# Kernel tuning notes

Measured on AMD Instinct MI355X. Metric: run time of the kernel, lower is better.

The kernel has to match this reference:

```python
import jax, jax.numpy as jnp
import numpy as np

N, IN_DIM, L, K, D = 131072, 128, 16, 8, 50
ENC_H, DEC_H, HEAD_H, DF = 64, 16, 64, 1.0


def setup_inputs() -> dict:
    key = jax.random.key(0)
    ks = jax.random.split(key, 20)
    s = lambda k, shape, fan: jax.random.normal(k, shape, jnp.float32) * (1.0 / np.sqrt(fan))
    return {
        "x": jax.random.normal(ks[0], (N, IN_DIM), jnp.float32),
        # encoder: in -> 64 -> 64 -> L
        "We1": s(ks[1], (IN_DIM, ENC_H), IN_DIM), "be1": jnp.zeros((ENC_H,), jnp.float32),
        "We2": s(ks[2], (ENC_H, ENC_H), ENC_H),   "be2": jnp.zeros((ENC_H,), jnp.float32),
        "We3": s(ks[3], (ENC_H, L), ENC_H),       "be3": jnp.zeros((L,), jnp.float32),
        # decoder: L -> 16 -> in
        "Wd1": s(ks[4], (L, DEC_H), L),           "bd1": jnp.zeros((DEC_H,), jnp.float32),
        "Wd2": s(ks[5], (DEC_H, IN_DIM), DEC_H),  "bd2": jnp.zeros((IN_DIM,), jnp.float32),
        # K per-cluster survival heads: (L+in) -> 64 -> num_durations
        "Wh1": s(ks[6], (K, L + IN_DIM, HEAD_H), L + IN_DIM), "bh1": jnp.zeros((K, HEAD_H), jnp.float32),
        "Wh2": s(ks[7], (K, HEAD_H, D), HEAD_H),              "bh2": jnp.zeros((K, D), jnp.float32),
        # cluster centers buffer
        "centers": jax.random.normal(ks[8], (K, L), jnp.float32) * 0.05,
    }


def _student_t_sim(z, centers, df):
    # z: [N, L], centers: [K, L] -> q: [N, K]
    dist2 = jnp.sum((z[:, None, :] - centers[None, :, :]) ** 2, axis=-1)
    logits = -0.5 * (df + 1.0) * jnp.log1p(dist2 / df)
    return jax.nn.softmax(logits, axis=1)


def reference(x, We1, be1, We2, be2, We3, be3, Wd1, bd1, Wd2, bd2,
              Wh1, bh1, Wh2, bh2, centers):
    relu = jax.nn.relu
    # encoder (eval mode: dropout off, non-variational)
    e = relu(x @ We1 + be1)
    e = relu(e @ We2 + be2)
    z = e @ We3 + be3                      # [N, L]
    q = _student_t_sim(z, centers, DF)     # [N, K]
    h = jnp.concatenate([z, x], axis=1)    # [N, L+in]
    # cluster-argmax routing to per-cluster heads: compute all K, select winner
    cluster_idx = jnp.argmax(q, axis=1)    # [N]
    h1 = relu(jnp.einsum("nf,kfh->nkh", h, Wh1) + bh1[None])   # [N, K, H]
    lg = jnp.einsum("nkh,khd->nkd", h1, Wh2) + bh2[None]       # [N, K, D]
    surv_logits = jnp.take_along_axis(lg, cluster_idx[:, None, None], axis=1)[:, 0]  # [N, D]
    # decoder + reconstruction loss per sample
    d = relu(z @ Wd1 + bd1)
    x_hat = d @ Wd2 + bd2                  # [N, in]
    rec_ps = jnp.mean((x_hat - x) ** 2, axis=1)
    kld = jnp.zeros((x.shape[0],), x.dtype)
    return z, q, surv_logits, x_hat, rec_ps, kld
```

## Files before the change

### kernel.cpp

```cpp
#include <hip/hip_runtime.h>

#define NS 131072
#define KC 8
typedef unsigned long long u64;

#define LD4(P) (*reinterpret_cast<const float4*>(&sm[(P)]))
#define ST4(P) (*reinterpret_cast<float4*>(&sm[(P)]))
#define GL4(P) (*reinterpret_cast<const float4*>(&(P)))

#define FMA4(ACCR, AV, B) do { \
  ACCR[0]=fmaf((AV),(B).x,ACCR[0]); ACCR[1]=fmaf((AV),(B).y,ACCR[1]); \
  ACCR[2]=fmaf((AV),(B).z,ACCR[2]); ACCR[3]=fmaf((AV),(B).w,ACCR[3]); } while(0)

#define K4(ACC, ABASE, ASTR, AK, BBASE, BSTR, JOFF, BK) do { \
  const float4 b0=LD4((BBASE)+((BK)*4+0)*(BSTR)+(JOFF)); \
  const float4 b1=LD4((BBASE)+((BK)*4+1)*(BSTR)+(JOFF)); \
  const float4 b2=LD4((BBASE)+((BK)*4+2)*(BSTR)+(JOFF)); \
  const float4 b3=LD4((BBASE)+((BK)*4+3)*(BSTR)+(JOFF)); \
  _Pragma("unroll") \
  for (int m_ = 0; m_ < 8; ++m_) { \
    const float4 av = LD4((ABASE)+(st+16*m_)*(ASTR)+(AK)*4); \
    FMA4(ACC[m_], av.x, b0); FMA4(ACC[m_], av.y, b1); \
    FMA4(ACC[m_], av.z, b2); FMA4(ACC[m_], av.w, b3); } \
} while(0)

#define INIT84(ACC, BPTR, OFF) do { \
  const float4 u_ = *reinterpret_cast<const float4*>(&(BPTR)[(OFF)]); \
  _Pragma("unroll") for (int m_=0;m_<8;++m_){ \
    ACC[m_][0]=u_.x; ACC[m_][1]=u_.y; ACC[m_][2]=u_.z; ACC[m_][3]=u_.w; } } while(0)

#define RELU84(ACC) do { _Pragma("unroll") for (int m_=0;m_<8;++m_) \
  { _Pragma("unroll") for (int j_=0;j_<4;++j_) ACC[m_][j_]=fmaxf(ACC[m_][j_],0.f); } } while(0)

#define WRITE_E(ACC) do { _Pragma("unroll") for (int m_=0;m_<8;++m_){ \
  ST4(AR + (st+16*m_)*68 + job) = \
    make_float4(ACC[m_][0],ACC[m_][1],ACC[m_][2],ACC[m_][3]); } } while(0)

#define STAGE_X() do { \
  ST4(AR + xr0*20 + xcc)     = rx0; \
  ST4(AR + xr0*20 + xcc + 4) = rx1; } while(0)

#define AR   0
#define WD1i 2560
#define WB   8704
#define SMW  9792

__global__ __launch_bounds__(256, 2) void k_enc(
    const float* __restrict__ x,
    const float* __restrict__ We1, const float* __restrict__ be1,
    const float* __restrict__ We2, const float* __restrict__ be2,
    const float* __restrict__ We3, const float* __restrict__ be3,
    const float* __restrict__ Wd1, const float* __restrict__ bd1,
    const float* __restrict__ Wd2, const float* __restrict__ bd2,
    const float* __restrict__ centers,
    float* __restrict__ out_z, float* __restrict__ out_q,
    float* __restrict__ xhat, float* __restrict__ rec, float* __restrict__ kld,
    int* __restrict__ cidx, int* __restrict__ counts)
{
    __shared__ float sm[SMW];
    const int t  = threadIdx.x;
    const int ot = t & 15, st = t >> 4;
    const int job = ot * 4;
    const int s0 = blockIdx.x * 128;
    const int xr0 = t >> 1, xcc = (t & 1) * 8;
    const int wr  = t >> 4, wc  = (t & 15) * 4;

    {
        float acc1[8][4];
        INIT84(acc1, be1, job);
        float4 rx0 = GL4(x[(size_t)(s0+xr0)*128 + xcc]);
        float4 rx1 = GL4(x[(size_t)(s0+xr0)*128 + xcc + 4]);
        float4 rw  = GL4(We1[(size_t)wr*64 + wc]);
        #pragma unroll 1
        for (int c = 0; c < 8; ++c) {
            __syncthreads();
            STAGE_X();
            ST4(WB + wr*68 + wc) = rw;
            __syncthreads();
            if (c < 7) {
                rx0 = GL4(x[(size_t)(s0+xr0)*128 + (c+1)*16 + xcc]);
                rx1 = GL4(x[(size_t)(s0+xr0)*128 + (c+1)*16 + xcc + 4]);
                rw  = GL4(We1[(size_t)((c+1)*16 + wr)*64 + wc]);
            }
            #pragma unroll
            for (int kc = 0; kc < 4; ++kc) K4(acc1, AR, 20, kc, WB, 68, job, kc);
        }
        __syncthreads();
        RELU84(acc1);
        WRITE_E(acc1);
    }

    {
        float acc2[8][4];
        INIT84(acc2, be2, job);
        float4 rw = GL4(We2[(size_t)wr*64 + wc]);
        #pragma unroll 1
        for (int c = 0; c < 4; ++c) {
            __syncthreads();
            ST4(WB + wr*68 + wc) = rw;
            __syncthreads();
            if (c < 3) rw = GL4(We2[(size_t)((c+1)*16 + wr)*64 + wc]);
            #pragma unroll
            for (int kc = 0; kc < 4; ++kc) K4(acc2, AR, 68, c*4 + kc, WB, 68, job, kc);
        }
        __syncthreads();
        RELU84(acc2);
        WRITE_E(acc2);
    }
    {   const int row = t >> 2, c4 = (t & 3) * 4;
        ST4(WB + row*16 + c4) = GL4(We3[(size_t)row*16 + c4]); }
    __syncthreads();

    float zac[8];
    {   const float b3v = be3[ot];
        #pragma unroll
        for (int m = 0; m < 8; ++m) zac[m] = b3v; }
    #pragma unroll 2
    for (int kc = 0; kc < 16; ++kc) {
        const float w0 = sm[WB + (kc*4+0)*16 + ot];
        const float w1 = sm[WB + (kc*4+1)*16 + ot];
        const float w2 = sm[WB + (kc*4+2)*16 + ot];
        const float w3 = sm[WB + (kc*4+3)*16 + ot];
        #pragma unroll
        for (int m = 0; m < 8; ++m) {
            const float4 av = LD4(AR + (st + 16*m)*68 + kc*4);
            float s = zac[m];
            s = fmaf(av.x, w0, s); s = fmaf(av.y, w1, s);
            s = fmaf(av.z, w2, s); s = fmaf(av.w, w3, s);
            zac[m] = s;
        }
    }
    #pragma unroll
    for (int m = 0; m < 8; ++m)
        out_z[(size_t)(s0 + st + 16*m)*16 + ot] = zac[m];
    __syncthreads();
    #pragma unroll
    for (int m = 0; m < 8; ++m) sm[AR + (st + 16*m)*20 + ot] = zac[m];
    ST4(WB + wr*68 + wc) = GL4(Wd2[(size_t)wr*128 + wc]);
    if (t < 64) ST4(WD1i + (t >> 2)*16 + (t & 3)*4) =
        GL4(Wd1[(t >> 2)*16 + (t & 3)*4]);
    __syncthreads();

    if (t < 128) {
        const float4 z0 = LD4(AR + t*20 + 0), z1 = LD4(AR + t*20 + 4);
        const float4 z2 = LD4(AR + t*20 + 8), z3 = LD4(AR + t*20 + 12);
        const float zz[16] = {z0.x,z0.y,z0.z,z0.w, z1.x,z1.y,z1.z,z1.w,
                              z2.x,z2.y,z2.z,z2.w, z3.x,z3.y,z3.z,z3.w};
        float d2[KC];
        #pragma unroll
        for (int k = 0; k < KC; ++k) {
            float acc = 0.f;
            #pragma unroll
            for (int l = 0; l < 16; ++l) {
                const float dl = zz[l] - centers[k*16 + l];
                acc = fmaf(dl, dl, acc);
            }
            d2[k] = acc;
        }
        float lgt[KC], ex[KC];
        float mm = -1e30f;
        #pragma unroll
        for (int k = 0; k < KC; ++k) { lgt[k] = -log1pf(d2[k]); mm = fmaxf(mm, lgt[k]); }
        float ssum = 0.f;
        #pragma unroll
        for (int k = 0; k < KC; ++k) { ex[k] = expf(lgt[k] - mm); ssum += ex[k]; }
        const float inv = 1.f / ssum;
        float4* oq = reinterpret_cast<float4*>(&out_q[(size_t)(s0 + t)*8]);
        oq[0] = make_float4(ex[0]*inv, ex[1]*inv, ex[2]*inv, ex[3]*inv);
        oq[1] = make_float4(ex[4]*inv, ex[5]*inv, ex[6]*inv, ex[7]*inv);
        int ci = 0; float best = d2[0];
        #pragma unroll
        for (int k = 1; k < KC; ++k) if (d2[k] < best) { best = d2[k]; ci = k; }
        cidx[s0 + t] = ci;
        #pragma unroll
        for (int k = 0; k < KC; ++k) {
            const u64 mk = __ballot(ci == k);
            if ((t & 63) == 0 && mk) atomicAdd(&counts[k], (int)__popcll(mk));
        }
        kld[s0 + t] = 0.f;
    }

    {
        float w[16];
        #pragma unroll
        for (int k = 0; k < 16; ++k) w[k] = sm[WD1i + k*16 + ot];
        const float bb = bd1[ot];
        float dac[8];
        #pragma unroll
        for (int m = 0; m < 8; ++m) {
            const int r = st + 16*m;
            float s = bb;
            #pragma unroll
            for (int kc = 0; kc < 4; ++kc) {
                const float4 av = LD4(AR + r*20 + kc*4);
                s = fmaf(av.x, w[kc*4+0], s); s = fmaf(av.y, w[kc*4+1], s);
                s = fmaf(av.z, w[kc*4+2], s); s = fmaf(av.w, w[kc*4+3], s);
            }
            dac[m] = fmaxf(s, 0.f);
        }
        __syncthreads();
        #pragma unroll
        for (int m = 0; m < 8; ++m) sm[AR + (st + 16*m)*20 + ot] = dac[m];
    }
    __syncthreads();

    float rp[8] = {0.f,0.f,0.f,0.f,0.f,0.f,0.f,0.f};
    float4 rw2 = GL4(Wd2[(size_t)wr*128 + 64 + wc]);
    {
        float accx[8][4];
        INIT84(accx, bd2, job);
        #pragma unroll
        for (int kc = 0; kc < 4; ++kc) K4(accx, AR, 20, kc, WB, 68, job, kc);
        #pragma unroll
        for (int m = 0; m < 8; ++m) {
            const int r = st + 16*m;
            const float4 xa = GL4(x[(size_t)(s0+r)*128 + job]);
            float df;
            df=accx[m][0]-xa.x; rp[m]=fmaf(df,df,rp[m]);
            df=accx[m][1]-xa.y; rp[m]=fmaf(df,df,rp[m]);
            df=accx[m][2]-xa.z; rp[m]=fmaf(df,df,rp[m]);
            df=accx[m][3]-xa.w; rp[m]=fmaf(df,df,rp[m]);
            *reinterpret_cast<float4*>(&xhat[(size_t)(s0+r)*128 + job]) =
                make_float4(accx[m][0],accx[m][1],accx[m][2],accx[m][3]);
        }
    }
    __syncthreads();
    ST4(WB + wr*68 + wc) = rw2;
    __syncthreads();
    {
        float accx[8][4];
        INIT84(accx, bd2, 64 + job);
        #pragma unroll
        for (int kc = 0; kc < 4; ++kc) K4(accx, AR, 20, kc, WB, 68, job, kc);
        #pragma unroll
        for (int m = 0; m < 8; ++m) {
            const int r = st + 16*m;
            const float4 xa = GL4(x[(size_t)(s0+r)*128 + 64 + job]);
            float df;
            df=accx[m][0]-xa.x; rp[m]=fmaf(df,df,rp[m]);
            df=accx[m][1]-xa.y; rp[m]=fmaf(df,df,rp[m]);
            df=accx[m][2]-xa.z; rp[m]=fmaf(df,df,rp[m]);
            df=accx[m][3]-xa.w; rp[m]=fmaf(df,df,rp[m]);
            *reinterpret_cast<float4*>(&xhat[(size_t)(s0+r)*128 + 64 + job]) =
                make_float4(accx[m][0],accx[m][1],accx[m][2],accx[m][3]);
        }
    }
    #pragma unroll
    for (int m = 0; m < 8; ++m) {
        float v = rp[m];
        v += __shfl_xor(v, 1); v += __shfl_xor(v, 2);
        v += __shfl_xor(v, 4); v += __shfl_xor(v, 8);
        if (ot == 0) rec[s0 + st + 16*m] = v * (1.f/128.f);
    }
}

__global__ void k_scan(const int* __restrict__ counts,
                       int* __restrict__ bases, int* __restrict__ cursors)
{
    if (threadIdx.x == 0) {
        int acc = 0;
        for (int k = 0; k < KC; ++k) { bases[k] = acc; cursors[k] = acc; acc += counts[k]; }
    }
}

__global__ __launch_bounds__(256) void k_scatter(
    const int* __restrict__ cidx, int* __restrict__ cursors, int* __restrict__ seg)
{
    const int s = blockIdx.x * 256 + threadIdx.x;
    const int lane = threadIdx.x & 63;
    const int ci = cidx[s];
    #pragma unroll
    for (int k = 0; k < KC; ++k) {
        const u64 mk = __ballot(ci == k);
        if (ci == k) {
            const int leader = __ffsll(mk) - 1;
            int base = 0;
            if (lane == leader) base = atomicAdd(&cursors[k], (int)__popcll(mk));
            base = __shfl(base, leader, 64);
            seg[base + (int)__popcll(mk & (((u64)1 << lane) - 1))] = s;
        }
    }
}

__global__ __launch_bounds__(256, 2) void k_heads(
    const float* __restrict__ x, const float* __restrict__ zread,
    const float* __restrict__ Wh1, const float* __restrict__ bh1,
    const float* __restrict__ Wh2, const float* __restrict__ bh2,
    const int* __restrict__ counts, const int* __restrict__ bases,
    const int* __restrict__ seg,
    float* __restrict__ surv)
{
    __shared__ float sm[SMW];
    __shared__ int idxs[128];
    const int t  = threadIdx.x;
    const int ot = t & 15, st = t >> 4;
    const int job = ot * 4;
    const int xr0 = t >> 1, xcc = (t & 1) * 8;
    const int wr  = t >> 4, wc  = (t & 15) * 4;

    int kk = -1, chunk = 0, pref = 0;
    #pragma unroll
    for (int q = 0; q < KC; ++q) {
        const int ck = (counts[q] + 127) >> 7;
        if (kk < 0) {
            if ((int)blockIdx.x < pref + ck) { kk = q; chunk = (int)blockIdx.x - pref; }
            pref += ck;
        }
    }
    if (kk < 0) return;
    kk    = __builtin_amdgcn_readfirstlane(kk);
    chunk = __builtin_amdgcn_readfirstlane(chunk);
    const int cnt  = __builtin_amdgcn_readfirstlane(counts[kk]);
    const int base = __builtin_amdgcn_readfirstlane(bases[kk]);

    if (t < 128) {
        const int i = chunk*128 + t;
        idxs[t] = seg[base + ((i < cnt) ? i : (cnt - 1))];
    }
    __syncthreads();
    const int irow = idxs[xr0];

    {
        float acc1[8][4];
        INIT84(acc1, bh1, (size_t)kk*64 + job);
        {
            ST4(AR + xr0*20 + xcc)     = GL4(zread[(size_t)irow*16 + xcc]);
            ST4(AR + xr0*20 + xcc + 4) = GL4(zread[(size_t)irow*16 + xcc + 4]);
            ST4(WB + wr*68 + wc) = GL4(Wh1[((size_t)kk*144 + wr)*64 + wc]); }
        __syncthreads();
        float4 rx0 = GL4(x[(size_t)irow*128 + xcc]);
        float4 rx1 = GL4(x[(size_t)irow*128 + xcc + 4]);
        float4 rw  = GL4(Wh1[((size_t)kk*144 + 16 + wr)*64 + wc]);
        #pragma unroll
        for (int kc = 0; kc < 4; ++kc) K4(acc1, AR, 20, kc, WB, 68, job, kc);
        #pragma unroll 1
        for (int c = 0; c < 8; ++c) {
            __syncthreads();
            STAGE_X();
            ST4(WB + wr*68 + wc) = rw;
            __syncthreads();
            if (c < 7) {
                rx0 = GL4(x[(size_t)irow*128 + (c+1)*16 + xcc]);
                rx1 = GL4(x[(size_t)irow*128 + (c+1)*16 + xcc + 4]);
                rw  = GL4(Wh1[((size_t)kk*144 + 16 + (c+1)*16 + wr)*64 + wc]);
            }
            #pragma unroll
            for (int kc = 0; kc < 4; ++kc) K4(acc1, AR, 20, kc, WB, 68, job, kc);
        }
        __syncthreads();
        RELU84(acc1);
        WRITE_E(acc1);
    }

    float acc2[8][4];
    {   float4 bz;
        bz.x = (job+0 < 50) ? bh2[(size_t)kk*50 + job+0] : 0.f;
        bz.y = (job+1 < 50) ? bh2[(size_t)kk*50 + job+1] : 0.f;
        bz.z = (job+2 < 50) ? bh2[(size_t)kk*50 + job+2] : 0.f;
        bz.w = (job+3 < 50) ? bh2[(size_t)kk*50 + job+3] : 0.f;
        #pragma unroll
        for (int m = 0; m < 8; ++m) {
            acc2[m][0] = bz.x; acc2[m][1] = bz.y;
            acc2[m][2] = bz.z; acc2[m][3] = bz.w;
        } }
    float4 rv;
    {   const int gk = wr;
        rv.x = (wc+0 < 50) ? Wh2[((size_t)kk*64 + gk)*50 + wc+0] : 0.f;
        rv.y = (wc+1 < 50) ? Wh2[((size_t)kk*64 + gk)*50 + wc+1] : 0.f;
        rv.z = (wc+2 < 50) ? Wh2[((size_t)kk*64 + gk)*50 + wc+2] : 0.f;
        rv.w = (wc+3 < 50) ? Wh2[((size_t)kk*64 + gk)*50 + wc+3] : 0.f; }
    #pragma unroll 1
    for (int c = 0; c < 4; ++c) {
        __syncthreads();
        ST4(WB + wr*68 + wc) = rv;
        __syncthreads();
        if (c < 3) {
            const int gk = (c+1)*16 + wr;
            rv.x = (wc+0 < 50) ? Wh2[((size_t)kk*64 + gk)*50 + wc+0] : 0.f;
            rv.y = (wc+1 < 50) ? Wh2[((size_t)kk*64 + gk)*50 + wc+1] : 0.f;
            rv.z = (wc+2 < 50) ? Wh2[((size_t)kk*64 + gk)*50 + wc+2] : 0.f;
            rv.w = (wc+3 < 50) ? Wh2[((size_t)kk*64 + gk)*50 + wc+3] : 0.f;
        }
        #pragma unroll
        for (int kc = 0; kc < 4; ++kc) K4(acc2, AR, 68, c*4 + kc, WB, 68, job, kc);
    }

    #pragma unroll
    for (int m = 0; m < 8; ++m) {
        const int r = st + 16*m;
        if (chunk*128 + r < cnt) {
            float* so = &surv[(size_t)idxs[r]*50 + job];
            if (ot < 12) {
                *reinterpret_cast<float2*>(&so[0]) = make_float2(acc2[m][0], acc2[m][1]);
                *reinterpret_cast<float2*>(&so[2]) = make_float2(acc2[m][2], acc2[m][3]);
            } else if (ot == 12) {
                *reinterpret_cast<float2*>(&so[0]) = make_float2(acc2[m][0], acc2[m][1]);
            }
        }
    }
}

extern "C" void kernel_launch(void* const* d_in, const int* in_sizes, int n_in,
                              void* d_out, int out_size, void* d_ws, size_t ws_size,
                              hipStream_t stream)
{
    const float* x   = (const float*)d_in[0];
    const float* We1 = (const float*)d_in[1];
    const float* be1 = (const float*)d_in[2];
    const float* We2 = (const float*)d_in[3];
    const float* be2 = (const float*)d_in[4];
    const float* We3 = (const float*)d_in[5];
    const float* be3 = (const float*)d_in[6];
    const float* Wd1 = (const float*)d_in[7];
    const float* bd1 = (const float*)d_in[8];
    const float* Wd2 = (const float*)d_in[9];
    const float* bd2 = (const float*)d_in[10];
    const float* Wh1 = (const float*)d_in[11];
    const float* bh1 = (const float*)d_in[12];
    const float* Wh2 = (const float*)d_in[13];
    const float* bh2 = (const float*)d_in[14];
    const float* cen = (const float*)d_in[15];
    float* out = (float*)d_out;

    float* out_z  = out;
    float* out_q  = out + (size_t)NS * 16;
    float* out_sv = out + (size_t)NS * 24;
    float* out_xh = out + (size_t)NS * 74;
    float* out_rc = out + (size_t)NS * 202;
    float* out_kl = out + (size_t)NS * 203;

    int* cidx    = (int*)d_ws;
    int* counts  = cidx + NS;
    int* bases   = counts + KC;
    int* cursors = bases + KC;
    int* seg     = cursors + KC;

    hipMemsetAsync(counts, 0, KC * sizeof(int), stream);

    k_enc<<<dim3(NS / 128), dim3(256), 0, stream>>>(
        x, We1, be1, We2, be2, We3, be3, Wd1, bd1, Wd2, bd2, cen,
        out_z, out_q, out_xh, out_rc, out_kl, cidx, counts);

    k_scan<<<dim3(1), dim3(64), 0, stream>>>(counts, bases, cursors);

    k_scatter<<<dim3(NS / 256), dim3(256), 0, stream>>>(cidx, cursors, seg);

    k_heads<<<dim3(NS / 128 + KC), dim3(256), 0, stream>>>(
        x, out_z, Wh1, bh1, Wh2, bh2, counts, bases, seg, out_sv);
}
```

Before: 447.0 us.

## Use single-wavefront blocks and read weights from global, dropping LDS weight staging

Both the encoder and head kernels now run 64-thread blocks that each handle 32 rows, instead of 256-thread blocks handling 128 rows. Weight tiles are no longer staged into shared memory; each lane loads weight float4s directly from global memory, relying on cache hits. Because each block is a single wavefront, every __syncthreads barrier is removed, and the head kernel's Wh2 loop is flattened. This cuts barrier stalls and LDS traffic, at the cost of global-load latency inside the inner FMA loops and more blocks re-reading the same weights.

Result: slower. 628.5 us (+40.6%).

```diff
diff --git a/kernel.cpp b/kernel.cpp
--- a/kernel.cpp
+++ b/kernel.cpp
@@ -7,19 +7,20 @@
 #define LD4(P) (*reinterpret_cast<const float4*>(&sm[(P)]))
 #define ST4(P) (*reinterpret_cast<float4*>(&sm[(P)]))
 #define GL4(P) (*reinterpret_cast<const float4*>(&(P)))
+#define GL2(P) (*reinterpret_cast<const float2*>(&(P)))
 
 #define FMA4(ACCR, AV, B) do { \
   ACCR[0]=fmaf((AV),(B).x,ACCR[0]); ACCR[1]=fmaf((AV),(B).y,ACCR[1]); \
   ACCR[2]=fmaf((AV),(B).z,ACCR[2]); ACCR[3]=fmaf((AV),(B).w,ACCR[3]); } while(0)
 
-#define K4(ACC, ABASE, ASTR, AK, BBASE, BSTR, JOFF, BK) do { \
-  const float4 b0=LD4((BBASE)+((BK)*4+0)*(BSTR)+(JOFF)); \
-  const float4 b1=LD4((BBASE)+((BK)*4+1)*(BSTR)+(JOFF)); \
-  const float4 b2=LD4((BBASE)+((BK)*4+2)*(BSTR)+(JOFF)); \
-  const float4 b3=LD4((BBASE)+((BK)*4+3)*(BSTR)+(JOFF)); \
+#define K4G(ACC, ABASE, ASTR, AK, BROWPTR, BSTR, JO) do { \
+  const float4 b0 = GL4((BROWPTR)[0*(BSTR) + (JO)]); \
+  const float4 b1 = GL4((BROWPTR)[1*(BSTR) + (JO)]); \
+  const float4 b2 = GL4((BROWPTR)[2*(BSTR) + (JO)]); \
+  const float4 b3 = GL4((BROWPTR)[3*(BSTR) + (JO)]); \
   _Pragma("unroll") \
   for (int m_ = 0; m_ < 8; ++m_) { \
-    const float4 av = LD4((ABASE)+(st+16*m_)*(ASTR)+(AK)*4); \
+    const float4 av = LD4((ABASE)+(st+4*m_)*(ASTR)+(AK)*4); \
     FMA4(ACC[m_], av.x, b0); FMA4(ACC[m_], av.y, b1); \
     FMA4(ACC[m_], av.z, b2); FMA4(ACC[m_], av.w, b3); } \
 } while(0)
@@ -33,19 +34,14 @@
   { _Pragma("unroll") for (int j_=0;j_<4;++j_) ACC[m_][j_]=fmaxf(ACC[m_][j_],0.f); } } while(0)
 
 #define WRITE_E(ACC) do { _Pragma("unroll") for (int m_=0;m_<8;++m_){ \
-  ST4(AR + (st+16*m_)*68 + job) = \
+  ST4(EA + (st+4*m_)*68 + job) = \
     make_float4(ACC[m_][0],ACC[m_][1],ACC[m_][2],ACC[m_][3]); } } while(0)
 
-#define STAGE_X() do { \
-  ST4(AR + xr0*20 + xcc)     = rx0; \
-  ST4(AR + xr0*20 + xcc + 4) = rx1; } while(0)
-
-#define AR   0
-#define WD1i 2560
-#define WB   8704
-#define SMW  9792
-
-__global__ __launch_bounds__(256, 2) void k_enc(
+#define XS  0
+#define EA  640
+#define SMW 2816
+
+__global__ __launch_bounds__(64, 4) void k_enc(
     const float* __restrict__ x,
     const float* __restrict__ We1, const float* __restrict__ be1,
     const float* __restrict__ We2, const float* __restrict__ be2,
@@ -58,58 +54,42 @@
     int* __restrict__ cidx, int* __restrict__ counts)
 {
     __shared__ float sm[SMW];
-    const int t  = threadIdx.x;
-    const int ot = t & 15, st = t >> 4;
+    const int l  = threadIdx.x;
+    const int ot = l & 15, st = l >> 4;
     const int job = ot * 4;
-    const int s0 = blockIdx.x * 128;
-    const int xr0 = t >> 1, xcc = (t & 1) * 8;
-    const int wr  = t >> 4, wc  = (t & 15) * 4;
-
-    {
-        float acc1[8][4];
-        INIT84(acc1, be1, job);
-        float4 rx0 = GL4(x[(size_t)(s0+xr0)*128 + xcc]);
-        float4 rx1 = GL4(x[(size_t)(s0+xr0)*128 + xcc + 4]);
-        float4 rw  = GL4(We1[(size_t)wr*64 + wc]);
+    const int s0 = blockIdx.x * 32;
+    const int xr = l >> 1, xcc = (l & 1) * 8;
+
+    float acc1[8][4];
+    INIT84(acc1, be1, job);
+    {
+        float4 rx0 = GL4(x[(size_t)(s0+xr)*128 + xcc]);
+        float4 rx1 = GL4(x[(size_t)(s0+xr)*128 + xcc + 4]);
         #pragma unroll 1
         for (int c = 0; c < 8; ++c) {
-            __syncthreads();
-            STAGE_X();
-            ST4(WB + wr*68 + wc) = rw;
-            __syncthreads();
+            ST4(XS + xr*20 + xcc)     = rx0;
+            ST4(XS + xr*20 + xcc + 4) = rx1;
             if (c < 7) {
-                rx0 = GL4(x[(size_t)(s0+xr0)*128 + (c+1)*16 + xcc]);
-                rx1 = GL4(x[(size_t)(s0+xr0)*128 + (c+1)*16 + xcc + 4]);
-                rw  = GL4(We1[(size_t)((c+1)*16 + wr)*64 + wc]);
+                rx0 = GL4(x[(size_t)(s0+xr)*128 + (c+1)*16 + xcc]);
+                rx1 = GL4(x[(size_t)(s0+xr)*128 + (c+1)*16 + xcc + 4]);
             }
             #pragma unroll
-            for (int kc = 0; kc < 4; ++kc) K4(acc1, AR, 20, kc, WB, 68, job, kc);
-        }
-        __syncthreads();
-        RELU84(acc1);
-        WRITE_E(acc1);
-    }
+            for (int kc = 0; kc < 4; ++kc)
+                K4G(acc1, XS, 20, kc, We1 + (size_t)(c*16 + kc*4)*64, 64, job);
+        }
+    }
+    RELU84(acc1);
+    WRITE_E(acc1);
 
     {
         float acc2[8][4];
         INIT84(acc2, be2, job);
-        float4 rw = GL4(We2[(size_t)wr*64 + wc]);
-        #pragma unroll 1
-        for (int c = 0; c < 4; ++c) {
-            __syncthreads();
-            ST4(WB + wr*68 + wc) = rw;
-            __syncthreads();
-            if (c < 3) rw = GL4(We2[(size_t)((c+1)*16 + wr)*64 + wc]);
-            #pragma unroll
-            for (int kc = 0; kc < 4; ++kc) K4(acc2, AR, 68, c*4 + kc, WB, 68, job, kc);
-        }
-        __syncthreads();
+        #pragma unroll 2
+        for (int kc = 0; kc < 16; ++kc)
+            K4G(acc2, EA, 68, kc, We2 + (size_t)(kc*4)*64, 64, job);
         RELU84(acc2);
         WRITE_E(acc2);
     }
-    {   const int row = t >> 2, c4 = (t & 3) * 4;
-        ST4(WB + row*16 + c4) = GL4(We3[(size_t)row*16 + c4]); }
-    __syncthreads();
 
     float zac[8];
     {   const float b3v = be3[ot];
@@ -117,13 +97,13 @@
         for (int m = 0; m < 8; ++m) zac[m] = b3v; }
     #pragma unroll 2
     for (int kc = 0; kc < 16; ++kc) {
-        const float w0 = sm[WB + (kc*4+0)*16 + ot];
-        const float w1 = sm[WB + (kc*4+1)*16 + ot];
-        const float w2 = sm[WB + (kc*4+2)*16 + ot];
-        const float w3 = sm[WB + (kc*4+3)*16 + ot];
-        #pragma unroll
-        for (int m = 0; m < 8; ++m) {
-            const float4 av = LD4(AR + (st + 16*m)*68 + kc*4);
+        const float w0 = We3[(kc*4+0)*16 + ot];
+        const float w1 = We3[(kc*4+1)*16 + ot];
+        const float w2 = We3[(kc*4+2)*16 + ot];
+        const float w3 = We3[(kc*4+3)*16 + ot];
+        #pragma unroll
+        for (int m = 0; m < 8; ++m) {
+            const float4 av = LD4(EA + (st + 4*m)*68 + kc*4);
             float s = zac[m];
             s = fmaf(av.x, w0, s); s = fmaf(av.y, w1, s);
             s = fmaf(av.z, w2, s); s = fmaf(av.w, w3, s);
@@ -132,18 +112,13 @@
     }
     #pragma unroll
     for (int m = 0; m < 8; ++m)
-        out_z[(size_t)(s0 + st + 16*m)*16 + ot] = zac[m];
-    __syncthreads();
-    #pragma unroll
-    for (int m = 0; m < 8; ++m) sm[AR + (st + 16*m)*20 + ot] = zac[m];
-    ST4(WB + wr*68 + wc) = GL4(Wd2[(size_t)wr*128 + wc]);
-    if (t < 64) ST4(WD1i + (t >> 2)*16 + (t & 3)*4) =
-        GL4(Wd1[(t >> 2)*16 + (t & 3)*4]);
-    __syncthreads();
-
-    if (t < 128) {
-        const float4 z0 = LD4(AR + t*20 + 0), z1 = LD4(AR + t*20 + 4);
-        const float4 z2 = LD4(AR + t*20 + 8), z3 = LD4(AR + t*20 + 12);
+        out_z[(size_t)(s0 + st + 4*m)*16 + ot] = zac[m];
+    #pragma unroll
+    for (int m = 0; m < 8; ++m) sm[XS + (st + 4*m)*20 + ot] = zac[m];
+
+    if (l < 32) {
+        const float4 z0 = LD4(XS + l*20 + 0), z1 = LD4(XS + l*20 + 4);
+        const float4 z2 = LD4(XS + l*20 + 8), z3 = LD4(XS + l*20 + 12);
         const float zz[16] = {z0.x,z0.y,z0.z,z0.w, z1.x,z1.y,z1.z,z1.w,
                               z2.x,z2.y,z2.z,z2.w, z3.x,z3.y,z3.z,z3.w};
         float d2[KC];
@@ -151,8 +126,8 @@
         for (int k = 0; k < KC; ++k) {
             float acc = 0.f;
             #pragma unroll
-            for (int l = 0; l < 16; ++l) {
-                const float dl = zz[l] - centers[k*16 + l];
+            for (int q = 0; q < 16; ++q) {
+                const float dl = zz[q] - centers[k*16 + q];
                 acc = fmaf(dl, dl, acc);
             }
             d2[k] = acc;
@@ -165,83 +140,61 @@
         #pragma unroll
         for (int k = 0; k < KC; ++k) { ex[k] = expf(lgt[k] - mm); ssum += ex[k]; }
         const float inv = 1.f / ssum;
-        float4* oq = reinterpret_cast<float4*>(&out_q[(size_t)(s0 + t)*8]);
+        float4* oq = reinterpret_cast<float4*>(&out_q[(size_t)(s0 + l)*8]);
         oq[0] = make_float4(ex[0]*inv, ex[1]*inv, ex[2]*inv, ex[3]*inv);
         oq[1] = make_float4(ex[4]*inv, ex[5]*inv, ex[6]*inv, ex[7]*inv);
         int ci = 0; float best = d2[0];
         #pragma unroll
         for (int k = 1; k < KC; ++k) if (d2[k] < best) { best = d2[k]; ci = k; }
-        cidx[s0 + t] = ci;
+        cidx[s0 + l] = ci;
         #pragma unroll
         for (int k = 0; k < KC; ++k) {
             const u64 mk = __ballot(ci == k);
-            if ((t & 63) == 0 && mk) atomicAdd(&counts[k], (int)__popcll(mk));
-        }
-        kld[s0 + t] = 0.f;
+            if (l == 0 && mk) atomicAdd(&counts[k], (int)__popcll(mk));
+        }
+        kld[s0 + l] = 0.f;
     }
 
     {
         float w[16];
         #pragma unroll
-        for (int k = 0; k < 16; ++k) w[k] = sm[WD1i + k*16 + ot];
+        for (int k = 0; k < 16; ++k) w[k] = Wd1[k*16 + ot];
         const float bb = bd1[ot];
         float dac[8];
         #pragma unroll
         for (int m = 0; m < 8; ++m) {
-            const int r = st + 16*m;
+            const int r = st + 4*m;
             float s = bb;
             #pragma unroll
             for (int kc = 0; kc < 4; ++kc) {
-                const float4 av = LD4(AR + r*20 + kc*4);
+                const float4 av = LD4(XS + r*20 + kc*4);
                 s = fmaf(av.x, w[kc*4+0], s); s = fmaf(av.y, w[kc*4+1], s);
                 s = fmaf(av.z, w[kc*4+2], s); s = fmaf(av.w, w[kc*4+3], s);
             }
             dac[m] = fmaxf(s, 0.f);
         }
-        __syncthreads();
-        #pragma unroll
-        for (int m = 0; m < 8; ++m) sm[AR + (st + 16*m)*20 + ot] = dac[m];
-    }
-    __syncthreads();
+        #pragma unroll
+        for (int m = 0; m < 8; ++m) sm[XS + (st + 4*m)*20 + ot] = dac[m];
+    }
 
     float rp[8] = {0.f,0.f,0.f,0.f,0.f,0.f,0.f,0.f};
-    float4 rw2 = GL4(Wd2[(size_t)wr*128 + 64 + wc]);
-    {
+    #pragma unroll
+    for (int h = 0; h < 2; ++h) {
         float accx[8][4];
-        INIT84(accx, bd2, job);
-        #pragma unroll
-        for (int kc = 0; kc < 4; ++kc) K4(accx, AR, 20, kc, WB, 68, job, kc);
-        #pragma unroll
-        for (int m = 0; m < 8; ++m) {
-            const int r = st + 16*m;
-            const float4 xa = GL4(x[(size_t)(s0+r)*128 + job]);
+        INIT84(accx, bd2, h*64 + job);
+        #pragma unroll
+        for (int kc = 0; kc < 4; ++kc)
+            K4G(accx, XS, 20, kc, Wd2 + (size_t)(kc*4)*128 + h*64, 128, job);
+        #pragma unroll
+        for (int m = 0; m < 8; ++m) {
+            const int r = st + 4*m;
+            const float4 xa = GL4(x[(size_t)(s0+r)*128 + h*64 + job]);
             float df;
             df=accx[m][0]-xa.x; rp[m]=fmaf(df,df,rp[m]);
             df=accx[m][1]-xa.y; rp[m]=fmaf(df,df,rp[m]);
             df=accx[m][2]-xa.z; rp[m]=fmaf(df,df,rp[m]);
             df=accx[m][3]-xa.w; rp[m]=fmaf(df,df,rp[m]);
-            *reinterpret_cast<float4*>(&xhat[(size_t)(s0+r)*128 + job]) =
-                make_float4(accx[m][0],accx[m][1],accx[m][2],accx[m][3]);
-        }
-    }
-    __syncthreads();
-    ST4(WB + wr*68 + wc) = rw2;
-    __syncthreads();
-    {
-        float accx[8][4];
-        INIT84(accx, bd2, 64 + job);
-        #pragma unroll
-        for (int kc = 0; kc < 4; ++kc) K4(accx, AR, 20, kc, WB, 68, job, kc);
-        #pragma unroll
-        for (int m = 0; m < 8; ++m) {
-            const int r = st + 16*m;
-            const float4 xa = GL4(x[(size_t)(s0+r)*128 + 64 + job]);
-            float df;
-            df=accx[m][0]-xa.x; rp[m]=fmaf(df,df,rp[m]);
-            df=accx[m][1]-xa.y; rp[m]=fmaf(df,df,rp[m]);
-            df=accx[m][2]-xa.z; rp[m]=fmaf(df,df,rp[m]);
-            df=accx[m][3]-xa.w; rp[m]=fmaf(df,df,rp[m]);
-            *reinterpret_cast<float4*>(&xhat[(size_t)(s0+r)*128 + 64 + job]) =
+            *reinterpret_cast<float4*>(&xhat[(size_t)(s0+r)*128 + h*64 + job]) =
                 make_float4(accx[m][0],accx[m][1],accx[m][2],accx[m][3]);
         }
     }
@@ -250,7 +203,7 @@
         float v = rp[m];
         v += __shfl_xor(v, 1); v += __shfl_xor(v, 2);
         v += __shfl_xor(v, 4); v += __shfl_xor(v, 8);
-        if (ot == 0) rec[s0 + st + 16*m] = v * (1.f/128.f);
+        if (ot == 0) rec[s0 + st + 4*m] = v * (1.f/128.f);
     }
 }
 
@@ -282,7 +235,7 @@
     }
 }
 
-__global__ __launch_bounds__(256, 2) void k_heads(
+__global__ __launch_bounds__(64, 4) void k_heads(
     const float* __restrict__ x, const float* __restrict__ zread,
     const float* __restrict__ Wh1, const float* __restrict__ bh1,
     const float* __restrict__ Wh2, const float* __restrict__ bh2,
@@ -291,17 +244,16 @@
     float* __restrict__ surv)
 {
     __shared__ float sm[SMW];
-    __shared__ int idxs[128];
-    const int t  = threadIdx.x;
-    const int ot = t & 15, st = t >> 4;
+    __shared__ int idxs[32];
+    const int l  = threadIdx.x;
+    const int ot = l & 15, st = l >> 4;
     const int job = ot * 4;
-    const int xr0 = t >> 1, xcc = (t & 1) * 8;
-    const int wr  = t >> 4, wc  = (t & 15) * 4;
+    const int xr = l >> 1, xcc = (l & 1) * 8;
 
     int kk = -1, chunk = 0, pref = 0;
     #pragma unroll
     for (int q = 0; q < KC; ++q) {
-        const int ck = (counts[q] + 127) >> 7;
+        const int ck = (counts[q] + 31) >> 5;
         if (kk < 0) {
             if ((int)blockIdx.x < pref + ck) { kk = q; chunk = (int)blockIdx.x - pref; }
             pref += ck;
@@ -313,82 +265,72 @@
     const int cnt  = __builtin_amdgcn_readfirstlane(counts[kk]);
     const int base = __builtin_amdgcn_readfirstlane(bases[kk]);
 
-    if (t < 128) {
-        const int i = chunk*128 + t;
-        idxs[t] = seg[base + ((i < cnt) ? i : (cnt - 1))];
-    }
-    __syncthreads();
-    const int irow = idxs[xr0];
-
-    {
-        float acc1[8][4];
-        INIT84(acc1, bh1, (size_t)kk*64 + job);
-        {
-            ST4(AR + xr0*20 + xcc)     = GL4(zread[(size_t)irow*16 + xcc]);
-            ST4(AR + xr0*20 + xcc + 4) = GL4(zread[(size_t)irow*16 + xcc + 4]);
-            ST4(WB + wr*68 + wc) = GL4(Wh1[((size_t)kk*144 + wr)*64 + wc]); }
-        __syncthreads();
+    if (l < 32) {
+        const int i = chunk*32 + l;
+        idxs[l] = seg[base + ((i < cnt) ? i : (cnt - 1))];
+    }
+    const int irow = idxs[xr];
+
+    float acc1[8][4];
+    INIT84(acc1, bh1, (size_t)kk*64 + job);
+    {
+        ST4(XS + xr*20 + xcc)     = GL4(zread[(size_t)irow*16 + xcc]);
+        ST4(XS + xr*20 + xcc + 4) = GL4(zread[(size_t)irow*16 + xcc + 4]);
+        #pragma unroll
+        for (int kc = 0; kc < 4; ++kc)
+            K4G(acc1, XS, 20, kc, Wh1 + ((size_t)kk*144 + kc*4)*64, 64, job);
         float4 rx0 = GL4(x[(size_t)irow*128 + xcc]);
         float4 rx1 = GL4(x[(size_t)irow*128 + xcc + 4]);
-        float4 rw  = GL4(Wh1[((size_t)kk*144 + 16 + wr)*64 + wc]);
-        #pragma unroll
-        for (int kc = 0; kc < 4; ++kc) K4(acc1, AR, 20, kc, WB, 68, job, kc);
         #pragma unroll 1
         for (int c = 0; c < 8; ++c) {
-            __syncthreads();
-            STAGE_X();
-            ST4(WB + wr*68 + wc) = rw;
-            __syncthreads();
+            ST4(XS + xr*20 + xcc)     = rx0;
+            ST4(XS + xr*20 + xcc + 4) = rx1;
             if (c < 7) {
                 rx0 = GL4(x[(size_t)irow*128 + (c+1)*16 + xcc]);
                 rx1 = GL4(x[(size_t)irow*128 + (c+1)*16 + xcc + 4]);
-                rw  = GL4(Wh1[((size_t)kk*144 + 16 + (c+1)*16 + wr)*64 + wc]);
             }
             #pragma unroll
-            for (int kc = 0; kc < 4; ++kc) K4(acc1, AR, 20, kc, WB, 68, job, kc);
-        }
-        __syncthreads();
-        RELU84(acc1);
-        WRITE_E(acc1);
-    }
+            for (int kc = 0; kc < 4; ++kc)
+                K4G(acc1, XS, 20, kc,
+                    Wh1 + ((size_t)kk*144 + 16 + c*16 + kc*4)*64, 64, job);
+        }
+    }
+    RELU84(acc1);
+    WRITE_E(acc1);
 
     float acc2[8][4];
-    {   float4 bz;
-        bz.x = (job+0 < 50) ? bh2[(size_t)kk*50 + job+0] : 0.f;
-        bz.y = (job+1 < 50) ? bh2[(size_t)kk*50 + job+1] : 0.f;
-        bz.z = (job+2 < 50) ? bh2[(size_t)kk*50 + job+2] : 0.f;
-        bz.w = (job+3 < 50) ? bh2[(size_t)kk*50 + job+3] : 0.f;
-        #pragma unroll
-        for (int m = 0; m < 8; ++m) {
-            acc2[m][0] = bz.x; acc2[m][1] = bz.y;
-            acc2[m][2] = bz.z; acc2[m][3] = bz.w;
-        } }
-    float4 rv;
-    {   const int gk = wr;
-        rv.x = (wc+0 < 50) ? Wh2[((size_t)kk*64 + gk)*50 + wc+0] : 0.f;
-        rv.y = (wc+1 < 50) ? Wh2[((size_t)kk*64 + gk)*50 + wc+1] : 0.f;
-        rv.z = (wc+2 < 50) ? Wh2[((size_t)kk*64 + gk)*50 + wc+2] : 0.f;
-        rv.w = (wc+3 < 50) ? Wh2[((size_t)kk*64 + gk)*50 + wc+3] : 0.f; }
-    #pragma unroll 1
-    for (int c = 0; c < 4; ++c) {
-        __syncthreads();
-        ST4(WB + wr*68 + wc) = rv;
-        __syncthreads();
-        if (c < 3) {
-            const int gk = (c+1)*16 + wr;
-            rv.x = (wc+0 < 50) ? Wh2[((size_t)kk*64 + gk)*50 + wc+0] : 0.f;
-            rv.y = (wc+1 < 50) ? Wh2[((size_t)kk*64 + gk)*50 + wc+1] : 0.f;
-            rv.z = (wc+2 < 50) ? Wh2[((size_t)kk*64 + gk)*50 + wc+2] : 0.f;
-            rv.w = (wc+3 < 50) ? Wh2[((size_t)kk*64 + gk)*50 + wc+3] : 0.f;
-        }
-        #pragma unroll
-        for (int kc = 0; kc < 4; ++kc) K4(acc2, AR, 68, c*4 + kc, WB, 68, job, kc);
-    }
+    {
+        #pragma unroll
+        for (int m = 0; m < 8; ++m) {
+            acc2[m][0] = (job+0 < 50) ? bh2[(size_t)kk*50 + job+0] : 0.f;
+            acc2[m][1] = (job+1 < 50) ? bh2[(size_t)kk*50 + job+1] : 0.f;
+            acc2[m][2] = (job+2 < 50) ? bh2[(size_t)kk*50 + job+2] : 0.f;
+            acc2[m][3] = (job+3 < 50) ? bh2[(size_t)kk*50 + job+3] : 0.f;
+        }
+    }
+    #define MKB(BV, KR) float4 BV; { \
+        const float* wp_ = Wh2 + ((size_t)kk*64 + (KR))*50; \
+        if (job < 50)     { const float2 p_ = GL2(wp_[job]);     BV.x = p_.x; BV.y = p_.y; } \
+        else              { BV.x = 0.f; BV.y = 0.f; } \
+        if (job + 2 < 50) { const float2 p_ = GL2(wp_[job + 2]); BV.z = p_.x; BV.w = p_.y; } \
+        else              { BV.z = 0.f; BV.w = 0.f; } }
+    #pragma unroll 2
+    for (int kc = 0; kc < 16; ++kc) {
+        MKB(b0, kc*4 + 0); MKB(b1, kc*4 + 1);
+        MKB(b2, kc*4 + 2); MKB(b3, kc*4 + 3);
+        #pragma unroll
+        for (int m = 0; m < 8; ++m) {
+            const float4 av = LD4(EA + (st + 4*m)*68 + kc*4);
+            FMA4(acc2[m], av.x, b0); FMA4(acc2[m], av.y, b1);
+            FMA4(acc2[m], av.z, b2); FMA4(acc2[m], av.w, b3);
+        }
+    }
+    #undef MKB
 
     #pragma unroll
     for (int m = 0; m < 8; ++m) {
-        const int r = st + 16*m;
-        if (chunk*128 + r < cnt) {
+        const int r = st + 4*m;
+        if (chunk*32 + r < cnt) {
             float* so = &surv[(size_t)idxs[r]*50 + job];
             if (ot < 12) {
                 *reinterpret_cast<float2*>(&so[0]) = make_float2(acc2[m][0], acc2[m][1]);
@@ -437,7 +379,7 @@
 
     hipMemsetAsync(counts, 0, KC * sizeof(int), stream);
 
-    k_enc<<<dim3(NS / 128), dim3(256), 0, stream>>>(
+    k_enc<<<dim3(NS / 32), dim3(64), 0, stream>>>(
         x, We1, be1, We2, be2, We3, be3, Wd1, bd1, Wd2, bd2, cen,
         out_z, out_q, out_xh, out_rc, out_kl, cidx, counts);
 
@@ -445,6 +387,6 @@
 
     k_scatter<<<dim3(NS / 256), dim3(256), 0, stream>>>(cidx, cursors, seg);
 
-    k_heads<<<dim3(NS / 128 + KC), dim3(256), 0, stream>>>(
+    k_heads<<<dim3(NS / 32 + KC), dim3(64), 0, stream>>>(
         x, out_z, Wh1, bh1, Wh2, bh2, counts, bases, seg, out_sv);
 }
```

## Rewrite per-cluster head GEMMs with bf16 MFMA on 64-row tiles

Applied to the files above, without the earlier changes.

Replaces the fp32 FMA-based per-cluster head kernel with a bf16 MFMA (16x16x32) implementation. Gathered input rows and weights are converted to bf16 and staged in shared memory, then both head layers run as matrix-core ops. Tiles shrink from 128 to 64 rows per block. An extra barrier is also added in the encoder before the We3 staging. This trades fp32 precision for bf16 on the head outputs, which may affect accuracy tolerance. Weight staging uses scalar strided global loads redone in every block.

Result: slower. 475.9 us (+6.5%).

```diff
diff --git a/kernel.cpp b/kernel.cpp
--- a/kernel.cpp
+++ b/kernel.cpp
@@ -3,6 +3,9 @@
 #define NS 131072
 #define KC 8
 typedef unsigned long long u64;
+
+typedef __attribute__((ext_vector_type(8))) short short8v;
+typedef __attribute__((ext_vector_type(4))) float f32x4;
 
 #define LD4(P) (*reinterpret_cast<const float4*>(&sm[(P)]))
 #define ST4(P) (*reinterpret_cast<float4*>(&sm[(P)]))
@@ -107,6 +110,7 @@
         RELU84(acc2);
         WRITE_E(acc2);
     }
+    __syncthreads();
     {   const int row = t >> 2, c4 = (t & 3) * 4;
         ST4(WB + row*16 + c4) = GL4(We3[(size_t)row*16 + c4]); }
     __syncthreads();
@@ -282,7 +286,22 @@
     }
 }
 
-__global__ __launch_bounds__(256, 2) void k_heads(
+#define XTH 0
+#define WTH 10752
+#define H1H 10752
+#define W2H 15360
+#define SMH 21504
+
+__device__ __forceinline__ unsigned short f2bf(float f) {
+    unsigned u = __float_as_uint(f);
+    u = (u + 0x7FFFu + ((u >> 16) & 1u)) >> 16;
+    return (unsigned short)u;
+}
+__device__ __forceinline__ unsigned pk2(float a, float b) {
+    return (unsigned)f2bf(a) | ((unsigned)f2bf(b) << 16);
+}
+
+__global__ __launch_bounds__(256, 1) void k_heads(
     const float* __restrict__ x, const float* __restrict__ zread,
     const float* __restrict__ Wh1, const float* __restrict__ bh1,
     const float* __restrict__ Wh2, const float* __restrict__ bh2,
@@ -290,18 +309,15 @@
     const int* __restrict__ seg,
     float* __restrict__ surv)
 {
-    __shared__ float sm[SMW];
-    __shared__ int idxs[128];
-    const int t  = threadIdx.x;
-    const int ot = t & 15, st = t >> 4;
-    const int job = ot * 4;
-    const int xr0 = t >> 1, xcc = (t & 1) * 8;
-    const int wr  = t >> 4, wc  = (t & 15) * 4;
+    __shared__ unsigned short smh[SMH];
+    __shared__ int idxs[64];
+    const int t = threadIdx.x;
+    const int w = t >> 6, l = t & 63;
 
     int kk = -1, chunk = 0, pref = 0;
     #pragma unroll
     for (int q = 0; q < KC; ++q) {
-        const int ck = (counts[q] + 127) >> 7;
+        const int ck = (counts[q] + 63) >> 6;
         if (kk < 0) {
             if ((int)blockIdx.x < pref + ck) { kk = q; chunk = (int)blockIdx.x - pref; }
             pref += ck;
@@ -313,88 +329,110 @@
     const int cnt  = __builtin_amdgcn_readfirstlane(counts[kk]);
     const int base = __builtin_amdgcn_readfirstlane(bases[kk]);
 
-    if (t < 128) {
-        const int i = chunk*128 + t;
+    if (t < 64) {
+        const int i = chunk*64 + t;
         idxs[t] = seg[base + ((i < cnt) ? i : (cnt - 1))];
     }
     __syncthreads();
-    const int irow = idxs[xr0];
-
-    {
-        float acc1[8][4];
-        INIT84(acc1, bh1, (size_t)kk*64 + job);
-        {
-            ST4(AR + xr0*20 + xcc)     = GL4(zread[(size_t)irow*16 + xcc]);
-            ST4(AR + xr0*20 + xcc + 4) = GL4(zread[(size_t)irow*16 + xcc + 4]);
-            ST4(WB + wr*68 + wc) = GL4(Wh1[((size_t)kk*144 + wr)*64 + wc]); }
-        __syncthreads();
-        float4 rx0 = GL4(x[(size_t)irow*128 + xcc]);
-        float4 rx1 = GL4(x[(size_t)irow*128 + xcc + 4]);
-        float4 rw  = GL4(Wh1[((size_t)kk*144 + 16 + wr)*64 + wc]);
-        #pragma unroll
-        for (int kc = 0; kc < 4; ++kc) K4(acc1, AR, 20, kc, WB, 68, job, kc);
+
+    {
+        const int r = t >> 2, q = t & 3;
+        const int idx = idxs[r];
+        const float* zp = zread + (size_t)idx * 16;
+        const float* xp = x + (size_t)idx * 128;
         #pragma unroll 1
-        for (int c = 0; c < 8; ++c) {
-            __syncthreads();
-            STAGE_X();
-            ST4(WB + wr*68 + wc) = rw;
-            __syncthreads();
-            if (c < 7) {
-                rx0 = GL4(x[(size_t)irow*128 + (c+1)*16 + xcc]);
-                rx1 = GL4(x[(size_t)irow*128 + (c+1)*16 + xcc + 4]);
-                rw  = GL4(Wh1[((size_t)kk*144 + 16 + (c+1)*16 + wr)*64 + wc]);
-            }
-            #pragma unroll
-            for (int kc = 0; kc < 4; ++kc) K4(acc1, AR, 20, kc, WB, 68, job, kc);
-        }
-        __syncthreads();
-        RELU84(acc1);
-        WRITE_E(acc1);
-    }
-
-    float acc2[8][4];
-    {   float4 bz;
-        bz.x = (job+0 < 50) ? bh2[(size_t)kk*50 + job+0] : 0.f;
-        bz.y = (job+1 < 50) ? bh2[(size_t)kk*50 + job+1] : 0.f;
-        bz.z = (job+2 < 50) ? bh2[(size_t)kk*50 + job+2] : 0.f;
-        bz.w = (job+3 < 50) ? bh2[(size_t)kk*50 + job+3] : 0.f;
-        #pragma unroll
-        for (int m = 0; m < 8; ++m) {
-            acc2[m][0] = bz.x; acc2[m][1] = bz.y;
-            acc2[m][2] = bz.z; acc2[m][3] = bz.w;
-        } }
-    float4 rv;
-    {   const int gk = wr;
-        rv.x = (wc+0 < 50) ? Wh2[((size_t)kk*64 + gk)*50 + wc+0] : 0.f;
-        rv.y = (wc+1 < 50) ? Wh2[((size_t)kk*64 + gk)*50 + wc+1] : 0.f;
-        rv.z = (wc+2 < 50) ? Wh2[((size_t)kk*64 + gk)*50 + wc+2] : 0.f;
-        rv.w = (wc+3 < 50) ? Wh2[((size_t)kk*64 + gk)*50 + wc+3] : 0.f; }
-    #pragma unroll 1
-    for (int c = 0; c < 4; ++c) {
-        __syncthreads();
-        ST4(WB + wr*68 + wc) = rv;
-        __syncthreads();
-        if (c < 3) {
-            const int gk = (c+1)*16 + wr;
-            rv.x = (wc+0 < 50) ? Wh2[((size_t)kk*64 + gk)*50 + wc+0] : 0.f;
-            rv.y = (wc+1 < 50) ? Wh2[((size_t)kk*64 + gk)*50 + wc+1] : 0.f;
-            rv.z = (wc+2 < 50) ? Wh2[((size_t)kk*64 + gk)*50 + wc+2] : 0.f;
-            rv.w = (wc+3 < 50) ? Wh2[((size_t)kk*64 + gk)*50 + wc+3] : 0.f;
-        }
-        #pragma unroll
-        for (int kc = 0; kc < 4; ++kc) K4(acc2, AR, 68, c*4 + kc, WB, 68, job, kc);
-    }
-
-    #pragma unroll
-    for (int m = 0; m < 8; ++m) {
-        const int r = st + 16*m;
-        if (chunk*128 + r < cnt) {
-            float* so = &surv[(size_t)idxs[r]*50 + job];
-            if (ot < 12) {
-                *reinterpret_cast<float2*>(&so[0]) = make_float2(acc2[m][0], acc2[m][1]);
-                *reinterpret_cast<float2*>(&so[2]) = make_float2(acc2[m][2], acc2[m][3]);
-            } else if (ot == 12) {
-                *reinterpret_cast<float2*>(&so[0]) = make_float2(acc2[m][0], acc2[m][1]);
+        for (int p = 0; p < 21; ++p) {
+            const int c = q*42 + 2*p;
+            const float f0 = (c   < 16) ? zp[c]   : ((c   < 144) ? xp[c-16]   : 0.f);
+            const float f1 = (c+1 < 16) ? zp[c+1] : ((c+1 < 144) ? xp[c+1-16] : 0.f);
+            *reinterpret_cast<unsigned*>(&smh[XTH + r*168 + c]) = pk2(f0, f1);
+        }
+        const float* wp = Wh1 + (size_t)kk * 144 * 64;
+        #pragma unroll 1
+        for (int p = 0; p < 21; ++p) {
+            const int k = q*42 + 2*p;
+            const float f0 = (k   < 144) ? wp[(size_t)k*64 + r]     : 0.f;
+            const float f1 = (k+1 < 144) ? wp[(size_t)(k+1)*64 + r] : 0.f;
+            *reinterpret_cast<unsigned*>(&smh[WTH + r*168 + k]) = pk2(f0, f1);
+        }
+    }
+    __syncthreads();
+
+    f32x4 acc[4];
+    {
+        const int col = l & 15;
+        #pragma unroll
+        for (int nt = 0; nt < 4; ++nt) {
+            const float b = bh1[(size_t)kk*64 + nt*16 + col];
+            acc[nt][0] = b; acc[nt][1] = b; acc[nt][2] = b; acc[nt][3] = b;
+        }
+        #pragma unroll
+        for (int ks = 0; ks < 5; ++ks) {
+            const short8v a = *reinterpret_cast<const short8v*>(
+                &smh[XTH + (16*w + (l & 15))*168 + ks*32 + (l >> 4)*8]);
+            #pragma unroll
+            for (int nt = 0; nt < 4; ++nt) {
+                const short8v b = *reinterpret_cast<const short8v*>(
+                    &smh[WTH + (nt*16 + (l & 15))*168 + ks*32 + (l >> 4)*8]);
+                acc[nt] = __builtin_amdgcn_mfma_f32_16x16x32_bf16(a, b, acc[nt], 0, 0, 0);
+            }
+        }
+    }
+    __syncthreads();
+
+    #pragma unroll
+    for (int nt = 0; nt < 4; ++nt) {
+        #pragma unroll
+        for (int j = 0; j < 4; ++j) {
+            const int row = 16*w + (l >> 4)*4 + j;
+            const int col = nt*16 + (l & 15);
+            smh[H1H + row*72 + col] = f2bf(fmaxf(acc[nt][j], 0.f));
+        }
+    }
+    {
+        const int n2 = t >> 2, q = t & 3;
+        const float* w2 = Wh2 + (size_t)kk * 64 * 50;
+        #pragma unroll
+        for (int p = 0; p < 8; ++p) {
+            const int k = q*16 + 2*p;
+            const float f0 = (n2 < 50) ? w2[(size_t)k*50 + n2]     : 0.f;
+            const float f1 = (n2 < 50) ? w2[(size_t)(k+1)*50 + n2] : 0.f;
+            *reinterpret_cast<unsigned*>(&smh[W2H + n2*72 + k]) = pk2(f0, f1);
+        }
+    }
+    __syncthreads();
+
+    f32x4 acc2[4];
+    {
+        const int col = l & 15;
+        #pragma unroll
+        for (int nt = 0; nt < 4; ++nt) {
+            const int c = nt*16 + col;
+            const float b = (c < 50) ? bh2[(size_t)kk*50 + c] : 0.f;
+            acc2[nt][0] = b; acc2[nt][1] = b; acc2[nt][2] = b; acc2[nt][3] = b;
+        }
+        #pragma unroll
+        for (int ks = 0; ks < 2; ++ks) {
+            const short8v a = *reinterpret_cast<const short8v*>(
+                &smh[H1H + (16*w + (l & 15))*72 + ks*32 + (l >> 4)*8]);
+            #pragma unroll
+            for (int nt = 0; nt < 4; ++nt) {
+                const short8v b = *reinterpret_cast<const short8v*>(
+                    &smh[W2H + (nt*16 + (l & 15))*72 + ks*32 + (l >> 4)*8]);
+                acc2[nt] = __builtin_amdgcn_mfma_f32_16x16x32_bf16(a, b, acc2[nt], 0, 0, 0);
+            }
+        }
+    }
+
+    #pragma unroll
+    for (int nt = 0; nt < 4; ++nt) {
+        const int col = nt*16 + (l & 15);
+        if (col < 50) {
+            #pragma unroll
+            for (int j = 0; j < 4; ++j) {
+                const int row = 16*w + (l >> 4)*4 + j;
+                if (chunk*64 + row < cnt)
+                    surv[(size_t)idxs[row]*50 + col] = acc2[nt][j];
             }
         }
     }
@@ -445,6 +483,6 @@
 
     k_scatter<<<dim3(NS / 256), dim3(256), 0, stream>>>(cidx, cursors, seg);
 
-    k_heads<<<dim3(NS / 128 + KC), dim3(256), 0, stream>>>(
+    k_heads<<<dim3(NS / 64 + KC), dim3(256), 0, stream>>>(
         x, out_z, Wh1, bh1, Wh2, bh2, counts, bases, seg, out_sv);
 }
```
